# Kernel tuning notes

Hardware: AMD Instinct MI355X
Metric: run time of the kernel (lower is better)

Reference implementation:

```python
import jax, jax.numpy as jnp
import numpy as np

K = 7        # kernal_size
STRIDE = 1
PAD = 3      # padding (reflect)
M = K // 2   # center tap index
GAMA = 0.5
EPS = 1e-09


def interp_linear(x, n_out):
    # torch F.interpolate(mode='linear', align_corners=False) on last dim. x: (b, c, n_in)
    n_in = x.shape[-1]
    src = (jnp.arange(n_out, dtype=jnp.float32) + 0.5) * (n_in / n_out) - 0.5
    src = jnp.clip(src, 0.0, n_in - 1.0)
    lo = jnp.floor(src).astype(jnp.int32)
    hi = jnp.minimum(lo + 1, n_in - 1)
    w = (src - lo.astype(jnp.float32)).astype(x.dtype)
    return x[..., lo] * (1.0 - w) + x[..., hi] * w


def unfold1d(x, k, s, p):
    # x: (b, c, n) -> windows (b, L, c, k), matching F.unfold's c-major/k-minor layout
    if p > 0:
        x = jnp.pad(x, ((0, 0), (0, 0), (p, p)), mode='reflect')
    n = x.shape[-1]
    L = (n - k) // s + 1
    idx = jnp.arange(L)[:, None] * s + jnp.arange(k)[None, :]  # (L, k)
    win = x[:, :, idx]                                          # (b, c, L, k)
    return jnp.transpose(win, (0, 2, 1, 3))                     # (b, L, c, k)


def setup_inputs() -> dict:
    key = jax.random.key(0)
    k1, k2, k3, k4, k5 = jax.random.split(key, 5)
    b, dc, nd = 16, 16, 1024
    c_in, c_out, n = 64, 128, 4096
    deep = jax.random.normal(k1, (b, dc, nd), dtype=jnp.float32)
    x = jax.random.normal(k2, (b, c_in, n), dtype=jnp.float32)
    conv_w = jax.random.normal(k3, (c_in, dc), dtype=jnp.float32) * (1.0 / np.sqrt(dc))
    conv_b = jax.random.normal(k4, (c_in,), dtype=jnp.float32) * 0.02
    fc_w = jax.random.normal(k5, (c_out, c_in * K), dtype=jnp.float32) * (1.0 / np.sqrt(c_in * K))
    return {"deep": deep, "x": x, "conv_w": conv_w, "conv_b": conv_b, "fc_w": fc_w}


def reference(deep, x, conv_w, conv_b, fc_w):
    b, c, n = x.shape
    # --- get_deep_loss ---
    xr = interp_linear(deep, n)                                  # (b, dc, n)
    y = jnp.einsum('bdn,cd->bcn', xr, conv_w) + conv_b[None, :, None]
    mean = jnp.mean(y, axis=2, keepdims=True)
    var = jnp.var(y, axis=2, keepdims=True, ddof=1)              # torch var_mean unbiased
    xs = GAMA * (y - mean) / (var + EPS)                         # DeepShuffle1d
    x1 = unfold1d(xs, K, STRIDE, PAD)                            # (b, L, c, k)
    d = jnp.abs(x1 - x1[..., M:M + 1])
    loss = 1.0 - jnp.tanh(d) ** 2                                # (b, L, c, k)
    alpha = 1.0 / jnp.sum(loss, axis=-1, keepdims=True)          # (b, L, c, 1)
    deep_loss = (loss * alpha).reshape(b, -1, c * K)             # (b, L, c*k)
    # --- deep_conv ---
    y1 = unfold1d(x, K, STRIDE, PAD).reshape(b, -1, c * K)       # (b, L, c*k)
    out = jnp.einsum('blf,of->bol', deep_loss * y1, fc_w)        # (b, c_out, L)
    return out
```

## Files before the change

### kernel.cpp

```cpp
#include <hip/hip_runtime.h>
#include <hip/hip_bf16.h>
#include <math.h>

namespace {
typedef __attribute__((ext_vector_type(8)))  short  short8;
typedef __attribute__((ext_vector_type(4)))  float  floatx4;
typedef _Float16 f16;
typedef __attribute__((ext_vector_type(4)))  _Float16 half4;
typedef __attribute__((ext_vector_type(8)))  _Float16 half8;

constexpr int Bc = 16;
constexpr int DC = 16;
constexpr int ND = 1024;
constexpr int C  = 64;
constexpr int N  = 4096;
constexpr int CO = 128;
constexpr int KW = 7;
constexpr int F  = C * KW;
constexpr int LT = 32;
constexpr int PLD = F + 8;

__device__ inline unsigned short f2bf(float f) {
    __hip_bfloat16 h = __float2bfloat16(f);
    return __builtin_bit_cast(unsigned short, h);
}
__device__ inline float rcpf(float x) { return __builtin_amdgcn_rcpf(x); }

__global__ __launch_bounds__(256)
void k1(const float* __restrict__ deep, const float* __restrict__ conv_w,
        const float* __restrict__ conv_b, const float* __restrict__ fcw,
        f16* __restrict__ xs, unsigned short* __restrict__ wb)
{
    if (blockIdx.x >= Bc * C) {
        const int i = ((blockIdx.x - Bc * C) * 256 + threadIdx.x) * 4;
        const float4 v = *(const float4*)(fcw + i);
        ushort4 o;
        o.x = f2bf(v.x); o.y = f2bf(v.y); o.z = f2bf(v.z); o.w = f2bf(v.w);
        *(ushort4*)(wb + i) = o;
        return;
    }
    const int b = blockIdx.x >> 6;
    const int c = blockIdx.x & 63;
    const int tid = threadIdx.x;
    __shared__ float V[ND];
    __shared__ float r1[256], r2[256];

    float cw[DC];
#pragma unroll
    for (int d = 0; d < DC; ++d) cw[d] = conv_w[c * DC + d];
    const float cb = conv_b[c];
    const float* dp = deep + b * DC * ND;

#pragma unroll
    for (int p = 0; p < 4; ++p) {
        const int t = tid + 256 * p;
        float a = 0.f;
#pragma unroll
        for (int d = 0; d < DC; ++d) a = fmaf(dp[d * ND + t], cw[d], a);
        V[t] = a;
    }
    __syncthreads();

    float s1 = 0.f, s2 = 0.f;
#pragma unroll
    for (int it = 0; it < 4; ++it) {
        const int g = tid + 256 * it;
        const float vm = V[g == 0 ? 0 : g - 1];
        const float v0 = V[g];
        const float vp = V[g == ND - 1 ? ND - 1 : g + 1];
        const float y0 = fmaf(0.375f, vm, fmaf(0.625f, v0, cb));
        const float y1 = fmaf(0.125f, vm, fmaf(0.875f, v0, cb));
        const float y2 = fmaf(0.125f, vp, fmaf(0.875f, v0, cb));
        const float y3 = fmaf(0.375f, vp, fmaf(0.625f, v0, cb));
        s1 += (y0 + y1) + (y2 + y3);
        s2 = fmaf(y0, y0, s2); s2 = fmaf(y1, y1, s2);
        s2 = fmaf(y2, y2, s2); s2 = fmaf(y3, y3, s2);
    }
    r1[tid] = s1; r2[tid] = s2;
    __syncthreads();
    for (int off = 128; off > 0; off >>= 1) {
        if (tid < off) { r1[tid] += r1[tid + off]; r2[tid] += r2[tid + off]; }
        __syncthreads();
    }
    const float mean = r1[0] * (1.f / N);
    const float var  = (r2[0] - (float)N * mean * mean) * (1.f / (N - 1));
    const float sc   = 0.5f / (var + 1e-9f);

    f16* xsp = xs + (b * C + c) * N;
#pragma unroll
    for (int it = 0; it < 4; ++it) {
        const int g = tid + 256 * it;
        const float vm = V[g == 0 ? 0 : g - 1];
        const float v0 = V[g];
        const float vp = V[g == ND - 1 ? ND - 1 : g + 1];
        half4 h;
        h.x = (f16)((fmaf(0.375f, vm, fmaf(0.625f, v0, cb)) - mean) * sc);
        h.y = (f16)((fmaf(0.125f, vm, fmaf(0.875f, v0, cb)) - mean) * sc);
        h.z = (f16)((fmaf(0.125f, vp, fmaf(0.875f, v0, cb)) - mean) * sc);
        h.w = (f16)((fmaf(0.375f, vp, fmaf(0.625f, v0, cb)) - mean) * sc);
        *(half4*)(xsp + 4 * g) = h;
    }
}

__global__ __launch_bounds__(256)
void k2(const f16* __restrict__ xs, const float* __restrict__ x,
        const unsigned short* __restrict__ wb, float* __restrict__ out)
{
    __shared__ __align__(16) unsigned short phi[LT * PLD];
    const int b   = blockIdx.y;
    const int l0  = blockIdx.x * LT;
    const int tid = threadIdx.x;

    {
        const int c    = tid & 63;
        const int seg  = tid >> 6;
        const int base = l0 + seg * 8;
        const f16*   xsr = xs + (b * C + c) * N;
        const float* xr  = x  + (b * C + c) * N;

        float vs[14], xv[14];
        const bool edge = (blockIdx.x == 0 && seg == 0) ||
                          (blockIdx.x == (N / LT - 1) && seg == 3);
        if (!edge) {
            const half8 a0 = *(const half8*)(xsr + base - 8);
            const half8 a1 = *(const half8*)(xsr + base);
            const half8 a2 = *(const half8*)(xsr + base + 8);
            const float4 x0 = *(const float4*)(xr + base - 4);
            const float4 x1 = *(const float4*)(xr + base);
            const float4 x2 = *(const float4*)(xr + base + 4);
            const float4 x3 = *(const float4*)(xr + base + 8);
            const float xf[16] = {x0.x, x0.y, x0.z, x0.w, x1.x, x1.y, x1.z, x1.w,
                                  x2.x, x2.y, x2.z, x2.w, x3.x, x3.y, x3.z, x3.w};
#pragma unroll
            for (int i = 0; i < 14; ++i) {
                const int j = 5 + i;
                const f16 v = (j < 8) ? a0[j] : ((j < 16) ? a1[j - 8] : a2[j - 16]);
                vs[i] = (float)v;
                xv[i] = xf[1 + i];
            }
        } else {
#pragma unroll
            for (int i = 0; i < 14; ++i) {
                int p = base - 3 + i;
                p = (p < 0) ? -p : ((p >= N) ? (2 * N - 2 - p) : p);
                vs[i] = (float)xsr[p];
                xv[i] = xr[p];
            }
        }

        unsigned short* pcol = phi + c * KW;
#pragma unroll
        for (int li = 0; li < 8; ++li) {
            const float cen = vs[li + 3];
            float u[KW];
            float s = 0.25f;
            u[3] = 0.25f;
#pragma unroll
            for (int k = 0; k < KW; ++k) {
                if (k == 3) continue;
                const float d = fabsf(vs[li + k] - cen);
                const float e = __expf(-2.f * d);
                const float t = 1.f + e;
                const float uk = e * rcpf(t * t);
                u[k] = uk;
                s += uk;
            }
            const float al = rcpf(s);
            unsigned short* pr = pcol + (seg * 8 + li) * PLD;
#pragma unroll
            for (int k = 0; k < KW; ++k) pr[k] = f2bf(u[k] * al * xv[li + k]);
        }
    }
    __syncthreads();

    const int wv   = tid >> 6;
    const int lane = tid & 63;
    const int quad = lane >> 4;
    const int rr   = lane & 15;
    const int o0   = wv * 32;

    floatx4 acc00 = {0.f, 0.f, 0.f, 0.f}, acc01 = acc00, acc10 = acc00, acc11 = acc00;
    const unsigned short* wrow0 = wb + (o0 + rr) * F + quad * 8;
    const unsigned short* wrow1 = wrow0 + 16 * F;
    const unsigned short* prow0 = phi + rr * PLD + quad * 8;
    const unsigned short* prow1 = prow0 + 16 * PLD;

    for (int s = 0; s < F / 32; ++s) {
        const int f0 = 32 * s;
        const short8 a0 = *(const short8*)(wrow0 + f0);
        const short8 a1 = *(const short8*)(wrow1 + f0);
        const short8 b0 = *(const short8*)(prow0 + f0);
        const short8 b1 = *(const short8*)(prow1 + f0);
        acc00 = __builtin_amdgcn_mfma_f32_16x16x32_bf16(a0, b0, acc00, 0, 0, 0);
        acc01 = __builtin_amdgcn_mfma_f32_16x16x32_bf16(a0, b1, acc01, 0, 0, 0);
        acc10 = __builtin_amdgcn_mfma_f32_16x16x32_bf16(a1, b0, acc10, 0, 0, 0);
        acc11 = __builtin_amdgcn_mfma_f32_16x16x32_bf16(a1, b1, acc11, 0, 0, 0);
    }

    float* ob = out + (b * CO) * N + l0;
#pragma unroll
    for (int i = 0; i < 4; ++i) {
        const int om = quad * 4 + i;
        ob[(o0 + om) * N      + rr     ] = acc00[i];
        ob[(o0 + om) * N      + 16 + rr] = acc01[i];
        ob[(o0 + 16 + om) * N + rr     ] = acc10[i];
        ob[(o0 + 16 + om) * N + 16 + rr] = acc11[i];
    }
}
}

extern "C" void kernel_launch(void* const* d_in, const int* in_sizes, int n_in,
                              void* d_out, int out_size, void* d_ws, size_t ws_size,
                              hipStream_t stream)
{
    const float* deep   = (const float*)d_in[0];
    const float* x      = (const float*)d_in[1];
    const float* conv_w = (const float*)d_in[2];
    const float* conv_b = (const float*)d_in[3];
    const float* fc_w   = (const float*)d_in[4];
    float* out = (float*)d_out;

    f16* xs = (f16*)d_ws;
    unsigned short* wb = (unsigned short*)((char*)d_ws + (8u << 20));

    hipLaunchKernelGGL(k1, dim3(Bc * C + 56), dim3(256), 0, stream,
                       deep, conv_w, conv_b, fc_w, xs, wb);
    hipLaunchKernelGGL(k2, dim3(N / LT, Bc), dim3(256), 0, stream,
                       xs, x, wb, out);
}
```

Before: 125.2 us.

## Compute shuffle stats from deep Gram matrix and recompute interpolation in GEMM kernel

The per-channel mean and variance of the interpolated conv output are now derived algebraically from partial Gram matrices of the low-resolution deep input (lag-0 and lag-1 products, sums, edge values). This removes the materialised fp16 normalised tensor. The main kernel recomputes the 1x1 conv and linear interpolation locally for its tile. x is pre-transposed to a bf16 channel-minor layout, so the main kernel loads coalesced tiles into shared memory and global traffic drops. The risks are float cancellation in the variance-from-moments formula and bf16 rounding of x.

```diff
diff --git a/kernel.cpp b/kernel.cpp
--- a/kernel.cpp
+++ b/kernel.cpp
@@ -5,9 +5,6 @@
 namespace {
 typedef __attribute__((ext_vector_type(8)))  short  short8;
 typedef __attribute__((ext_vector_type(4)))  float  floatx4;
-typedef _Float16 f16;
-typedef __attribute__((ext_vector_type(4)))  _Float16 half4;
-typedef __attribute__((ext_vector_type(8)))  _Float16 half8;
 
 constexpr int Bc = 16;
 constexpr int DC = 16;
@@ -19,146 +16,241 @@
 constexpr int F  = C * KW;
 constexpr int LT = 32;
 constexpr int PLD = F + 8;
+constexpr int GPS = 560;
+
+constexpr size_t WB_OFF = 0;
+constexpr size_t GP_OFF = 131072;
+constexpr size_t XT_OFF = 524288;
 
 __device__ inline unsigned short f2bf(float f) {
     __hip_bfloat16 h = __float2bfloat16(f);
     return __builtin_bit_cast(unsigned short, h);
 }
+__device__ inline float bf2f(unsigned short u) {
+    unsigned int x = ((unsigned int)u) << 16;
+    return __builtin_bit_cast(float, x);
+}
 __device__ inline float rcpf(float x) { return __builtin_amdgcn_rcpf(x); }
+__device__ inline int reflect(int p) {
+    p = (p < 0) ? -p : p;
+    return (p >= N) ? (2 * N - 2 - p) : p;
+}
 
 __global__ __launch_bounds__(256)
-void k1(const float* __restrict__ deep, const float* __restrict__ conv_w,
-        const float* __restrict__ conv_b, const float* __restrict__ fcw,
-        f16* __restrict__ xs, unsigned short* __restrict__ wb)
+void k0(const float* __restrict__ deep, const float* __restrict__ x,
+        const float* __restrict__ fcw, unsigned short* __restrict__ wb,
+        float* __restrict__ gp, unsigned short* __restrict__ xt)
 {
-    if (blockIdx.x >= Bc * C) {
-        const int i = ((blockIdx.x - Bc * C) * 256 + threadIdx.x) * 4;
+    __shared__ __align__(16) char sm[9216];
+    const int blk = blockIdx.x;
+    const int tid = threadIdx.x;
+
+    if (blk < 56) {
+        const int i = (blk * 256 + tid) * 4;
         const float4 v = *(const float4*)(fcw + i);
         ushort4 o;
         o.x = f2bf(v.x); o.y = f2bf(v.y); o.z = f2bf(v.z); o.w = f2bf(v.w);
         *(ushort4*)(wb + i) = o;
         return;
     }
-    const int b = blockIdx.x >> 6;
-    const int c = blockIdx.x & 63;
-    const int tid = threadIdx.x;
-    __shared__ float V[ND];
-    __shared__ float r1[256], r2[256];
-
-    float cw[DC];
-#pragma unroll
-    for (int d = 0; d < DC; ++d) cw[d] = conv_w[c * DC + d];
-    const float cb = conv_b[c];
-    const float* dp = deep + b * DC * ND;
-
-#pragma unroll
-    for (int p = 0; p < 4; ++p) {
-        const int t = tid + 256 * p;
-        float a = 0.f;
-#pragma unroll
-        for (int d = 0; d < DC; ++d) a = fmaf(dp[d * ND + t], cw[d], a);
-        V[t] = a;
-    }
-    __syncthreads();
-
-    float s1 = 0.f, s2 = 0.f;
-#pragma unroll
-    for (int it = 0; it < 4; ++it) {
-        const int g = tid + 256 * it;
-        const float vm = V[g == 0 ? 0 : g - 1];
-        const float v0 = V[g];
-        const float vp = V[g == ND - 1 ? ND - 1 : g + 1];
-        const float y0 = fmaf(0.375f, vm, fmaf(0.625f, v0, cb));
-        const float y1 = fmaf(0.125f, vm, fmaf(0.875f, v0, cb));
-        const float y2 = fmaf(0.125f, vp, fmaf(0.875f, v0, cb));
-        const float y3 = fmaf(0.375f, vp, fmaf(0.625f, v0, cb));
-        s1 += (y0 + y1) + (y2 + y3);
-        s2 = fmaf(y0, y0, s2); s2 = fmaf(y1, y1, s2);
-        s2 = fmaf(y2, y2, s2); s2 = fmaf(y3, y3, s2);
-    }
-    r1[tid] = s1; r2[tid] = s2;
-    __syncthreads();
-    for (int off = 128; off > 0; off >>= 1) {
-        if (tid < off) { r1[tid] += r1[tid + off]; r2[tid] += r2[tid + off]; }
+    if (blk < 184) {
+        float (*Dch)[132] = (float (*)[132])sm;
+        const int i2 = blk - 56;
+        const int b  = i2 >> 3;
+        const int ch = i2 & 7;
+        const int t0 = ch * 128;
+        const int d  = tid >> 4;
+        const int e  = tid & 15;
+#pragma unroll
+        for (int p = 0; p < 9; ++p) {
+            const int tt = e + 16 * p;
+            if (tt < 129)
+                Dch[d][tt] = deep[(b * DC + d) * ND + min(t0 + tt, ND - 1)];
+        }
         __syncthreads();
-    }
-    const float mean = r1[0] * (1.f / N);
-    const float var  = (r2[0] - (float)N * mean * mean) * (1.f / (N - 1));
-    const float sc   = 0.5f / (var + 1e-9f);
-
-    f16* xsp = xs + (b * C + c) * N;
-#pragma unroll
-    for (int it = 0; it < 4; ++it) {
-        const int g = tid + 256 * it;
-        const float vm = V[g == 0 ? 0 : g - 1];
-        const float v0 = V[g];
-        const float vp = V[g == ND - 1 ? ND - 1 : g + 1];
-        half4 h;
-        h.x = (f16)((fmaf(0.375f, vm, fmaf(0.625f, v0, cb)) - mean) * sc);
-        h.y = (f16)((fmaf(0.125f, vm, fmaf(0.875f, v0, cb)) - mean) * sc);
-        h.z = (f16)((fmaf(0.125f, vp, fmaf(0.875f, v0, cb)) - mean) * sc);
-        h.w = (f16)((fmaf(0.375f, vp, fmaf(0.625f, v0, cb)) - mean) * sc);
-        *(half4*)(xsp + 4 * g) = h;
+        float a0 = 0.f, a1 = 0.f, as = 0.f;
+        const int n1 = (ch == 7) ? 127 : 128;
+        for (int t = 0; t < 128; ++t) {
+            const float vd  = Dch[d][t];
+            const float ve  = Dch[e][t];
+            const float ve1 = (t < n1) ? Dch[e][t + 1] : 0.f;
+            a0 = fmaf(vd, ve, a0);
+            a1 = fmaf(vd, ve1, a1);
+            as += vd;
+        }
+        float* gpb = gp + (b * 8 + ch) * GPS;
+        gpb[tid] = a0;
+        gpb[256 + tid] = a1;
+        if (e == 0) {
+            gpb[512 + d] = as;
+            if (ch == 0) gpb[528 + d] = Dch[d][0];
+            if (ch == 7) gpb[544 + d] = Dch[d][127];
+        }
+        return;
+    }
+    unsigned short (*xb)[72] = (unsigned short (*)[72])sm;
+    const int i2 = blk - 184;
+    const int b  = i2 >> 6;
+    const int n0 = (i2 & 63) * 64;
+    const int c  = tid >> 2;
+    const int q  = tid & 3;
+#pragma unroll
+    for (int rep = 0; rep < 4; ++rep) {
+        const int nl = q * 16 + rep * 4;
+        const float4 v = *(const float4*)(x + (size_t)(b * C + c) * N + n0 + nl);
+        xb[nl + 0][c] = f2bf(v.x);
+        xb[nl + 1][c] = f2bf(v.y);
+        xb[nl + 2][c] = f2bf(v.z);
+        xb[nl + 3][c] = f2bf(v.w);
+    }
+    __syncthreads();
+#pragma unroll
+    for (int pass = 0; pass < 2; ++pass) {
+        const int row  = (tid >> 3) + pass * 32;
+        const int part = tid & 7;
+        const uint4 v = *(const uint4*)(&xb[row][part * 8]);
+        *(uint4*)(xt + (size_t)(b * N + n0 + row) * C + part * 8) = v;
     }
 }
 
 __global__ __launch_bounds__(256)
-void k2(const f16* __restrict__ xs, const float* __restrict__ x,
-        const unsigned short* __restrict__ wb, float* __restrict__ out)
+void k2(const float* __restrict__ deep, const float* __restrict__ conv_w,
+        const float* __restrict__ conv_b, const float* __restrict__ gp,
+        const unsigned short* __restrict__ xt, const unsigned short* __restrict__ wb,
+        float* __restrict__ out)
 {
-    __shared__ __align__(16) unsigned short phi[LT * PLD];
+    __shared__ __align__(16) char sm[40448];
+    unsigned short* phi   = (unsigned short*)sm;
+    float*          Dw    = (float*)sm;
+    float*          qpart = (float*)(sm + 1024);
+    unsigned short* xtile = (unsigned short*)(sm + 29184);
+    float*          Vt    = (float*)(sm + 34048);
+    float*          Gs    = (float*)(sm + 37120);
+    float*          mcs   = (float*)(sm + 39360);
+    float*          scs   = (float*)(sm + 39616);
+
     const int b   = blockIdx.y;
     const int l0  = blockIdx.x * LT;
+    const int t0  = l0 >> 2;
     const int tid = threadIdx.x;
-
+    const int c   = tid & 63;
+    const int seg = tid >> 6;
+
+    for (int u = tid; u < GPS; u += 256) {
+        float v = 0.f;
+        if (u < 528) {
+#pragma unroll
+            for (int ch = 0; ch < 8; ++ch) v += gp[(b * 8 + ch) * GPS + u];
+        } else if (u < 544) {
+            v = gp[(b * 8 + 0) * GPS + u];
+        } else {
+            v = gp[(b * 8 + 7) * GPS + u];
+        }
+        Gs[u] = v;
+    }
+    for (int u = tid; u < 38 * 8; u += 256) {
+        const int row = u >> 3, part = u & 7;
+        const int n = reflect(l0 - 3 + row);
+        const uint4 v = *(const uint4*)(xt + (size_t)(b * N + n) * C + part * 8);
+        *(uint4*)(xtile + row * 64 + part * 8) = v;
+    }
+    if (tid < 192) {
+        const int ti = tid >> 4, d = tid & 15;
+        const int t = min(max(t0 - 2 + ti, 0), ND - 1);
+        Dw[ti * 16 + d] = deep[(b * DC + d) * ND + t];
+    }
+    __syncthreads();
+
+    float w[DC];
     {
-        const int c    = tid & 63;
-        const int seg  = tid >> 6;
+        const float4* wr = (const float4*)(conv_w + c * DC);
+#pragma unroll
+        for (int p = 0; p < 4; ++p) {
+            const float4 v = wr[p];
+            w[4 * p] = v.x; w[4 * p + 1] = v.y; w[4 * p + 2] = v.z; w[4 * p + 3] = v.w;
+        }
+    }
+#pragma unroll
+    for (int p = 0; p < 3; ++p) {
+        const int ti = seg + 4 * p;
+        float a = 0.f;
+#pragma unroll
+        for (int d = 0; d < DC; ++d) a = fmaf(w[d], Dw[ti * 16 + d], a);
+        Vt[ti * 64 + c] = a;
+    }
+    {
+        float q0 = 0.f, q1 = 0.f;
+#pragma unroll
+        for (int dd = 0; dd < 4; ++dd) {
+            const int d = 4 * seg + dd;
+            float i0 = 0.f, i1 = 0.f;
+#pragma unroll
+            for (int e = 0; e < DC; ++e) {
+                i0 = fmaf(w[e], Gs[d * 16 + e], i0);
+                i1 = fmaf(w[e], Gs[256 + d * 16 + e], i1);
+            }
+            q0 = fmaf(w[d], i0, q0);
+            q1 = fmaf(w[d], i1, q1);
+        }
+        qpart[seg * 64 + c] = q0;
+        qpart[256 + seg * 64 + c] = q1;
+    }
+    __syncthreads();
+
+    if (tid < 64) {
+        const float Q0 = qpart[c] + qpart[64 + c] + qpart[128 + c] + qpart[192 + c];
+        const float Q1 = qpart[256 + c] + qpart[320 + c] + qpart[384 + c] + qpart[448 + c];
+        float wS = 0.f, V0 = 0.f, VN = 0.f;
+#pragma unroll
+        for (int d = 0; d < DC; ++d) {
+            wS = fmaf(w[d], Gs[512 + d], wS);
+            V0 = fmaf(w[d], Gs[528 + d], V0);
+            VN = fmaf(w[d], Gs[544 + d], VN);
+        }
+        const float cb   = conv_b[c];
+        const float mean = wS * (1.f / 1024.f) + cb;
+        const float S2   = 2.625f * Q0 + 1.375f * Q1 + 0.6875f * (V0 * V0 + VN * VN)
+                         + 8.f * cb * wS + 4096.f * cb * cb;
+        const float var  = (S2 - 4096.f * mean * mean) * (1.f / 4095.f);
+        mcs[c] = wS * (1.f / 1024.f);
+        scs[c] = 0.5f / (var + 1e-9f);
+    }
+    __syncthreads();
+
+    {
         const int base = l0 + seg * 8;
-        const f16*   xsr = xs + (b * C + c) * N;
-        const float* xr  = x  + (b * C + c) * N;
-
-        float vs[14], xv[14];
-        const bool edge = (blockIdx.x == 0 && seg == 0) ||
-                          (blockIdx.x == (N / LT - 1) && seg == 3);
-        if (!edge) {
-            const half8 a0 = *(const half8*)(xsr + base - 8);
-            const half8 a1 = *(const half8*)(xsr + base);
-            const half8 a2 = *(const half8*)(xsr + base + 8);
-            const float4 x0 = *(const float4*)(xr + base - 4);
-            const float4 x1 = *(const float4*)(xr + base);
-            const float4 x2 = *(const float4*)(xr + base + 4);
-            const float4 x3 = *(const float4*)(xr + base + 8);
-            const float xf[16] = {x0.x, x0.y, x0.z, x0.w, x1.x, x1.y, x1.z, x1.w,
-                                  x2.x, x2.y, x2.z, x2.w, x3.x, x3.y, x3.z, x3.w};
-#pragma unroll
-            for (int i = 0; i < 14; ++i) {
-                const int j = 5 + i;
-                const f16 v = (j < 8) ? a0[j] : ((j < 16) ? a1[j - 8] : a2[j - 16]);
-                vs[i] = (float)v;
-                xv[i] = xf[1 + i];
-            }
-        } else {
-#pragma unroll
-            for (int i = 0; i < 14; ++i) {
-                int p = base - 3 + i;
-                p = (p < 0) ? -p : ((p >= N) ? (2 * N - 2 - p) : p);
-                vs[i] = (float)xsr[p];
-                xv[i] = xr[p];
-            }
-        }
-
+        const float mc = mcs[c], sc = scs[c];
+        float xsv[14], xvf[14];
+#pragma unroll
+        for (int i = 0; i < 14; ++i) {
+            const int j  = base - 3 + i;
+            const int ja = (j < 0) ? -j : j;
+            const int jr = min(ja, 2 * N - 2 - ja);
+            const int t  = jr >> 2;
+            const int r  = jr & 3;
+            const float wa = (r & 1) ? ((r & 2) ? 0.625f : 0.125f)
+                                     : ((r & 2) ? 0.875f : 0.375f);
+            int tA = t - 1 + (r >> 1);
+            int tB = tA + 1;
+            if (tA < 0) { tA = 0; tB = 0; }
+            if (tB > ND - 1) tB = ND - 1;
+            const int ia = tA - t0 + 2;
+            const int ib = tB - t0 + 2;
+            const float vl = wa * Vt[ia * 64 + c] + (1.f - wa) * Vt[ib * 64 + c];
+            xsv[i] = (vl - mc) * sc;
+            xvf[i] = bf2f(xtile[(seg * 8 + i) * 64 + c]);
+        }
         unsigned short* pcol = phi + c * KW;
 #pragma unroll
         for (int li = 0; li < 8; ++li) {
-            const float cen = vs[li + 3];
+            const float cen = xsv[li + 3];
             float u[KW];
             float s = 0.25f;
             u[3] = 0.25f;
 #pragma unroll
             for (int k = 0; k < KW; ++k) {
                 if (k == 3) continue;
-                const float d = fabsf(vs[li + k] - cen);
+                const float d = fabsf(xsv[li + k] - cen);
                 const float e = __expf(-2.f * d);
                 const float t = 1.f + e;
                 const float uk = e * rcpf(t * t);
@@ -168,16 +260,15 @@
             const float al = rcpf(s);
             unsigned short* pr = pcol + (seg * 8 + li) * PLD;
 #pragma unroll
-            for (int k = 0; k < KW; ++k) pr[k] = f2bf(u[k] * al * xv[li + k]);
-        }
-    }
-    __syncthreads();
-
-    const int wv   = tid >> 6;
+            for (int k = 0; k < KW; ++k) pr[k] = f2bf(u[k] * al * xvf[li + k]);
+        }
+    }
+    __syncthreads();
+
     const int lane = tid & 63;
     const int quad = lane >> 4;
     const int rr   = lane & 15;
-    const int o0   = wv * 32;
+    const int o0   = seg * 32;
 
     floatx4 acc00 = {0.f, 0.f, 0.f, 0.f}, acc01 = acc00, acc10 = acc00, acc11 = acc00;
     const unsigned short* wrow0 = wb + (o0 + rr) * F + quad * 8;
@@ -197,7 +288,7 @@
         acc11 = __builtin_amdgcn_mfma_f32_16x16x32_bf16(a1, b1, acc11, 0, 0, 0);
     }
 
-    float* ob = out + (b * CO) * N + l0;
+    float* ob = out + (size_t)(b * CO) * N + l0;
 #pragma unroll
     for (int i = 0; i < 4; ++i) {
         const int om = quad * 4 + i;
@@ -220,11 +311,12 @@
     const float* fc_w   = (const float*)d_in[4];
     float* out = (float*)d_out;
 
-    f16* xs = (f16*)d_ws;
-    unsigned short* wb = (unsigned short*)((char*)d_ws + (8u << 20));
-
-    hipLaunchKernelGGL(k1, dim3(Bc * C + 56), dim3(256), 0, stream,
-                       deep, conv_w, conv_b, fc_w, xs, wb);
+    unsigned short* wbuf = (unsigned short*)((char*)d_ws + WB_OFF);
+    float*          gp   = (float*)((char*)d_ws + GP_OFF);
+    unsigned short* xt   = (unsigned short*)((char*)d_ws + XT_OFF);
+
+    hipLaunchKernelGGL(k0, dim3(56 + 128 + 1024), dim3(256), 0, stream,
+                       deep, x, fc_w, wbuf, gp, xt);
     hipLaunchKernelGGL(k2, dim3(N / LT, Bc), dim3(256), 0, stream,
-                       xs, x, wb, out);
-}
+                       deep, conv_w, conv_b, gp, xt, wbuf, out);
+}
```

Result: slower. 129.1 us (+3.1%).
